# Kernel optimization log

Hardware: AMD Instinct MI355X
Metric: run time of the kernel (lower is better)

## Reference

```python
import jax, jax.numpy as jnp
import numpy as np

Y_SCALE = 0.01  # fixed weight quantization scale (q_scale of the int8 weights)


def setup_inputs() -> dict:
    key = jax.random.key(0)
    kx, kw, kb = jax.random.split(key, 3)
    B, S, IN, OUT = 4, 2048, 4096, 4096
    x = jax.random.normal(kx, (B, S, IN), dtype=jnp.float32)
    # int8 quantized weights, stored transposed as (in_features, out_features)
    weight_q = jax.random.randint(kw, (IN, OUT), -128, 128, dtype=jnp.int32)
    bias = jax.random.normal(kb, (OUT,), dtype=jnp.float32)
    return {"x": x, "weight_q": weight_q, "bias": bias}


def reference(x, weight_q, bias):
    # Per-batch-sample dynamic activation scale: max(|x_i|)/128 over each [S, IN] slice
    x_scale = jnp.max(jnp.abs(x), axis=(1, 2), keepdims=True) / 128.0  # [B,1,1]
    # int8 quantize: round + clip
    xq = jnp.clip(jnp.round(x / x_scale), -128, 127).astype(jnp.int8)  # [B,S,IN]
    wq = weight_q.astype(jnp.int8)                                      # [IN,OUT]
    c = jax.lax.dot_general(
        xq, wq,
        dimension_numbers=(((2,), (0,)), ((), ())),
        preferred_element_type=jnp.int32,
    )  # [B,S,OUT]
    # dequantize and bias-add
    y = c.astype(jnp.float32) * (x_scale * Y_SCALE)
    return y + bias
```

## Files before the change

kernel.cpp:

```cpp
#include <hip/hip_runtime.h>
#include <stdint.h>

#define K_DIM 4096
#define N_DIM 4096
#define M_DIM 8192
#define S_ROWS 2048
#define NT 32

typedef int v4i __attribute__((ext_vector_type(4)));

__device__ __forceinline__ void gload16(const void* g, void* l) {
    __builtin_amdgcn_global_load_lds(
        (const __attribute__((address_space(1))) unsigned int*)g,
        (__attribute__((address_space(3))) unsigned int*)l, 16, 0, 0);
}

__device__ __forceinline__ void barrier() {
    asm volatile("" ::: "memory");
    __builtin_amdgcn_s_barrier();
    asm volatile("" ::: "memory");
}

__global__ void prep1_kernel(const float* __restrict__ x, unsigned* __restrict__ amax,
                             const int* __restrict__ wq, char* __restrict__ wt) {
    __shared__ unsigned lds[64 * 17];
    if (blockIdx.x < 4096) {
        int b = blockIdx.x >> 10;
        int bx = blockIdx.x & 1023;
        const float4* xb = (const float4*)(x + (size_t)b * S_ROWS * K_DIM);
        int tid = bx * 256 + threadIdx.x;
        const int stride = 1024 * 256;
        float m = 0.f;
#pragma unroll
        for (int i = 0; i < 8; ++i) {
            float4 v = xb[tid + i * stride];
            m = fmaxf(m, fmaxf(fmaxf(fabsf(v.x), fabsf(v.y)),
                               fmaxf(fabsf(v.z), fabsf(v.w))));
        }
#pragma unroll
        for (int off = 32; off; off >>= 1)
            m = fmaxf(m, __shfl_xor(m, off));
        float* red = (float*)lds;
        if ((threadIdx.x & 63) == 0) red[threadIdx.x >> 6] = m;
        __syncthreads();
        if (threadIdx.x == 0) {
            m = fmaxf(fmaxf(red[0], red[1]), fmaxf(red[2], red[3]));
            atomicMax(&amax[b], __float_as_uint(m));
        }
    } else {
        int wb = blockIdx.x - 4096;
        int n0 = (wb & 63) * 64;
        int k0 = (wb >> 6) * 64;
        int t = threadIdx.x;
        int c = t & 63;
        int g = t >> 6;
#pragma unroll
        for (int rep = 0; rep < 4; ++rep) {
            int kb = g * 16 + rep * 4;
            int v0 = wq[(size_t)(k0 + kb + 0) * N_DIM + n0 + c];
            int v1 = wq[(size_t)(k0 + kb + 1) * N_DIM + n0 + c];
            int v2 = wq[(size_t)(k0 + kb + 2) * N_DIM + n0 + c];
            int v3 = wq[(size_t)(k0 + kb + 3) * N_DIM + n0 + c];
            lds[c * 17 + (kb >> 2)] =
                (v0 & 255) | ((v1 & 255) << 8) | ((v2 & 255) << 16) | ((v3 & 255) << 24);
        }
        __syncthreads();
        int row = t >> 2;
        int ch = t & 3;
        uint4 o;
        o.x = lds[row * 17 + ch * 4 + 0];
        o.y = lds[row * 17 + ch * 4 + 1];
        o.z = lds[row * 17 + ch * 4 + 2];
        o.w = lds[row * 17 + ch * 4 + 3];
        *(uint4*)(wt + (size_t)(n0 + row) * K_DIM + k0 + ch * 16) = o;
    }
}

__global__ void quant_kernel(const float* __restrict__ x,
                             const unsigned* __restrict__ amax,
                             char* __restrict__ xq) {
    size_t gid = (size_t)blockIdx.x * 256 + threadIdx.x;
    size_t base = gid * 16;
    int b = (int)(base >> 23);
    float inv = 128.0f / __uint_as_float(amax[b]);
    const float4* xs = (const float4*)(x + base);
    unsigned parts[4];
#pragma unroll
    for (int i = 0; i < 4; ++i) {
        float4 v = xs[i];
        int q0 = max(-128, min(127, (int)rintf(v.x * inv)));
        int q1 = max(-128, min(127, (int)rintf(v.y * inv)));
        int q2 = max(-128, min(127, (int)rintf(v.z * inv)));
        int q3 = max(-128, min(127, (int)rintf(v.w * inv)));
        parts[i] = (q0 & 255) | ((q1 & 255) << 8) | ((q2 & 255) << 16) | ((q3 & 255) << 24);
    }
    *(uint4*)(xq + base) = make_uint4(parts[0], parts[1], parts[2], parts[3]);
}

__global__ __launch_bounds__(512, 2) void gemm8_kernel(
    const char* __restrict__ A, const char* __restrict__ Bt,
    const float* __restrict__ bias, const unsigned* __restrict__ amax,
    float* __restrict__ out) {
    __shared__ char sm[131072];
    const int t = threadIdx.x;
    const int l = t & 63;
    const int w = t >> 6;
    const int wm = w >> 2;
    const int wn = w & 3;
    const int rb = l & 15;
    const int sg = l >> 4;

    int bid = blockIdx.x;
    int swz = (bid & 7) * 64 + (bid >> 3);
    int mt = swz >> 4, nt = swz & 15;
    const size_t m0 = (size_t)mt * 256;
    const size_t n0 = (size_t)nt * 256;

    const int s0 = (sg ^ (rb & 7)) << 4;
    const int s1 = s0 ^ 64;
    const int baseA = (wm * 128 + rb) * 128;
    const int baseB = 32768 + (wn * 64 + rb) * 128;

    v4i acc[8][4];
#pragma unroll
    for (int i = 0; i < 8; ++i)
#pragma unroll
        for (int j = 0; j < 4; ++j) acc[i][j] = (v4i){0, 0, 0, 0};

#define ST_FULL(tt)                                                          \
    if ((tt) < NT) {                                                         \
        char* lb = sm + (((tt) & 1) << 16);                                  \
        const char* ga = A + m0 * K_DIM + (size_t)(tt) * 128;                \
        const char* gb = Bt + n0 * K_DIM + (size_t)(tt) * 128;               \
        _Pragma("unroll")                                                    \
        for (int j = 0; j < 4; ++j) {                                        \
            int p = j * 512 + t;                                             \
            int r = p >> 3, sl = p & 7;                                      \
            int s = sl ^ (r & 7);                                            \
            gload16(ga + (size_t)r * K_DIM + s * 16, lb + p * 16);           \
        }                                                                    \
        _Pragma("unroll")                                                    \
        for (int j = 0; j < 4; ++j) {                                        \
            int p = j * 512 + t;                                             \
            int r = p >> 3, sl = p & 7;                                      \
            int s = sl ^ (r & 7);                                            \
            gload16(gb + (size_t)r * K_DIM + s * 16, lb + 32768 + p * 16);   \
        }                                                                    \
    }

#define MFMA_PAIR(accrow, afrag)                                             \
    _Pragma("unroll")                                                        \
    for (int ni = 0; ni < 4; ++ni)                                           \
        _Pragma("unroll")                                                    \
        for (int ks = 0; ks < 2; ++ks)                                       \
            acc[accrow][ni] = __builtin_amdgcn_mfma_i32_16x16x64_i8(         \
                afrag[ks], bF[ni][ks], acc[accrow][ni], 0, 0, 0);

    ST_FULL(0);

    v4i aP[2][2], bF[4][2];

    for (int i = 0; i < NT; ++i) {
        const char* pb = sm + ((i & 1) << 16);
        const char* pA0 = pb + baseA + s0;
        const char* pA1 = pb + baseA + s1;
        const char* pB0 = pb + baseB + s0;
        const char* pB1 = pb + baseB + s1;

        barrier();
        ST_FULL(i + 1);
        if (i == NT - 1) { asm volatile("s_waitcnt vmcnt(0)" ::: "memory"); }
        else             { asm volatile("s_waitcnt vmcnt(8)" ::: "memory"); }
        barrier();

#pragma unroll
        for (int ni = 0; ni < 4; ++ni) {
            bF[ni][0] = *(const v4i*)(pB0 + ni * 2048);
            bF[ni][1] = *(const v4i*)(pB1 + ni * 2048);
        }
        aP[0][0] = *(const v4i*)(pA0 + 0 * 2048); aP[0][1] = *(const v4i*)(pA1 + 0 * 2048);
        aP[1][0] = *(const v4i*)(pA0 + 1 * 2048); aP[1][1] = *(const v4i*)(pA1 + 1 * 2048);
        __builtin_amdgcn_s_setprio(1);
        MFMA_PAIR(0, aP[0]); MFMA_PAIR(1, aP[1]);
        aP[0][0] = *(const v4i*)(pA0 + 2 * 2048); aP[0][1] = *(const v4i*)(pA1 + 2 * 2048);
        aP[1][0] = *(const v4i*)(pA0 + 3 * 2048); aP[1][1] = *(const v4i*)(pA1 + 3 * 2048);
        MFMA_PAIR(2, aP[0]); MFMA_PAIR(3, aP[1]);
        aP[0][0] = *(const v4i*)(pA0 + 0 * 2048 + 8192); aP[0][1] = *(const v4i*)(pA1 + 0 * 2048 + 8192);
        aP[1][0] = *(const v4i*)(pA0 + 1 * 2048 + 8192); aP[1][1] = *(const v4i*)(pA1 + 1 * 2048 + 8192);
        MFMA_PAIR(4, aP[0]); MFMA_PAIR(5, aP[1]);
        aP[0][0] = *(const v4i*)(pA0 + 2 * 2048 + 8192); aP[0][1] = *(const v4i*)(pA1 + 2 * 2048 + 8192);
        aP[1][0] = *(const v4i*)(pA0 + 3 * 2048 + 8192); aP[1][1] = *(const v4i*)(pA1 + 3 * 2048 + 8192);
        MFMA_PAIR(6, aP[0]); MFMA_PAIR(7, aP[1]);
        __builtin_amdgcn_s_setprio(0);
    }

    float scale = __uint_as_float(amax[m0 >> 11]) * (1.0f / 128.0f) * 0.01f;
    float bv[4];
#pragma unroll
    for (int ni = 0; ni < 4; ++ni) bv[ni] = bias[n0 + wn * 64 + ni * 16 + rb];
#pragma unroll
    for (int mi = 0; mi < 8; ++mi) {
#pragma unroll
        for (int rg = 0; rg < 4; ++rg) {
            size_t row = m0 + wm * 128 + mi * 16 + sg * 4 + rg;
            float* orow = out + row * N_DIM + n0 + wn * 64 + rb;
#pragma unroll
            for (int ni = 0; ni < 4; ++ni)
                orow[ni * 16] = (float)acc[mi][ni][rg] * scale + bv[ni];
        }
    }
#undef ST_FULL
#undef MFMA_PAIR
}

extern "C" void kernel_launch(void* const* d_in, const int* in_sizes, int n_in,
                              void* d_out, int out_size, void* d_ws, size_t ws_size,
                              hipStream_t stream) {
    const float* x = (const float*)d_in[0];
    const int* wq = (const int*)d_in[1];
    const float* bias = (const float*)d_in[2];
    float* out = (float*)d_out;

    unsigned* amax = (unsigned*)d_ws;
    char* xq = (char*)d_ws + 256;
    char* wt = (char*)d_ws + 256 + (size_t)M_DIM * K_DIM;

    hipMemsetAsync(d_ws, 0, 16, stream);

    prep1_kernel<<<dim3(8192), 256, 0, stream>>>(x, amax, wq, wt);
    quant_kernel<<<8192, 256, 0, stream>>>(x, amax, xq);
    gemm8_kernel<<<dim3(512), 512, 0, stream>>>(xq, wt, bias, amax, out);
}
```

Measured before the change: 225.2 us.

## Pre-swizzle weights into MFMA fragment layout and load B directly to registers

The weight transpose kernel now writes B in a fragment-packed layout, so each lane can load its MFMA B operands straight from global memory into registers. This removes B from LDS, which halves shared memory to 64KB, and double-buffers B in registers (bP/bQ) across a two-step unrolled loop. The block-to-tile mapping is changed so each XCD covers two N tiles across all M. The cost is higher register pressure and full vmcnt(0) waits each step, which may expose global-load latency that was previously hidden.

Result: slower. 229.9 us (+2.1%).

```diff
diff --git a/kernel.cpp b/kernel.cpp
--- a/kernel.cpp
+++ b/kernel.cpp
@@ -20,6 +20,7 @@
     __builtin_amdgcn_s_barrier();
     asm volatile("" ::: "memory");
 }
+
 
 __global__ void prep1_kernel(const float* __restrict__ x, unsigned* __restrict__ amax,
                              const int* __restrict__ wq, char* __restrict__ wt) {
@@ -50,17 +51,17 @@
     } else {
         int wb = blockIdx.x - 4096;
         int n0 = (wb & 63) * 64;
-        int k0 = (wb >> 6) * 64;
+        int k0b = (wb >> 6) * 64;
         int t = threadIdx.x;
         int c = t & 63;
         int g = t >> 6;
 #pragma unroll
         for (int rep = 0; rep < 4; ++rep) {
             int kb = g * 16 + rep * 4;
-            int v0 = wq[(size_t)(k0 + kb + 0) * N_DIM + n0 + c];
-            int v1 = wq[(size_t)(k0 + kb + 1) * N_DIM + n0 + c];
-            int v2 = wq[(size_t)(k0 + kb + 2) * N_DIM + n0 + c];
-            int v3 = wq[(size_t)(k0 + kb + 3) * N_DIM + n0 + c];
+            int v0 = wq[(size_t)(k0b + kb + 0) * N_DIM + n0 + c];
+            int v1 = wq[(size_t)(k0b + kb + 1) * N_DIM + n0 + c];
+            int v2 = wq[(size_t)(k0b + kb + 2) * N_DIM + n0 + c];
+            int v3 = wq[(size_t)(k0b + kb + 3) * N_DIM + n0 + c];
             lds[c * 17 + (kb >> 2)] =
                 (v0 & 255) | ((v1 & 255) << 8) | ((v2 & 255) << 16) | ((v3 & 255) << 24);
         }
@@ -72,7 +73,11 @@
         o.y = lds[row * 17 + ch * 4 + 1];
         o.z = lds[row * 17 + ch * 4 + 2];
         o.w = lds[row * 17 + ch * 4 + 3];
-        *(uint4*)(wt + (size_t)(n0 + row) * K_DIM + k0 + ch * 16) = o;
+        int n = n0 + row;
+        int k0 = k0b + ch * 16;
+        size_t dst = ((size_t)(n >> 4) * 64 + (k0 >> 6)) * 1024 +
+                     (size_t)((n & 15) + ((k0 >> 4) & 3) * 16) * 16;
+        *(uint4*)(wt + dst) = o;
     }
 }
 
@@ -101,7 +106,7 @@
     const char* __restrict__ A, const char* __restrict__ Bt,
     const float* __restrict__ bias, const unsigned* __restrict__ amax,
     float* __restrict__ out) {
-    __shared__ char sm[131072];
+    __shared__ char sm[65536];
     const int t = threadIdx.x;
     const int l = t & 63;
     const int w = t >> 6;
@@ -111,15 +116,18 @@
     const int sg = l >> 4;
 
     int bid = blockIdx.x;
-    int swz = (bid & 7) * 64 + (bid >> 3);
-    int mt = swz >> 4, nt = swz & 15;
+    int xcd = bid & 7;
+    int idx = bid >> 3;
+    int nt = (xcd << 1) | (idx & 1);
+    int mt = idx >> 1;
     const size_t m0 = (size_t)mt * 256;
     const size_t n0 = (size_t)nt * 256;
 
     const int s0 = (sg ^ (rb & 7)) << 4;
     const int s1 = s0 ^ 64;
     const int baseA = (wm * 128 + rb) * 128;
-    const int baseB = 32768 + (wn * 64 + rb) * 128;
+
+    const char* bBase = Bt + (((size_t)(n0 >> 4) + wn * 4) * 64) * 1024 + l * 16;
 
     v4i acc[8][4];
 #pragma unroll
@@ -127,11 +135,10 @@
 #pragma unroll
         for (int j = 0; j < 4; ++j) acc[i][j] = (v4i){0, 0, 0, 0};
 
-#define ST_FULL(tt)                                                          \
+#define ST_A(tt)                                                             \
     if ((tt) < NT) {                                                         \
-        char* lb = sm + (((tt) & 1) << 16);                                  \
+        char* lb = sm + (((tt) & 1) << 15);                                  \
         const char* ga = A + m0 * K_DIM + (size_t)(tt) * 128;                \
-        const char* gb = Bt + n0 * K_DIM + (size_t)(tt) * 128;               \
         _Pragma("unroll")                                                    \
         for (int j = 0; j < 4; ++j) {                                        \
             int p = j * 512 + t;                                             \
@@ -139,59 +146,72 @@
             int s = sl ^ (r & 7);                                            \
             gload16(ga + (size_t)r * K_DIM + s * 16, lb + p * 16);           \
         }                                                                    \
-        _Pragma("unroll")                                                    \
-        for (int j = 0; j < 4; ++j) {                                        \
-            int p = j * 512 + t;                                             \
-            int r = p >> 3, sl = p & 7;                                      \
-            int s = sl ^ (r & 7);                                            \
-            gload16(gb + (size_t)r * K_DIM + s * 16, lb + 32768 + p * 16);   \
-        }                                                                    \
-    }
-
-#define MFMA_PAIR(accrow, afrag)                                             \
-    _Pragma("unroll")                                                        \
-    for (int ni = 0; ni < 4; ++ni)                                           \
-        _Pragma("unroll")                                                    \
-        for (int ks = 0; ks < 2; ++ks)                                       \
-            acc[accrow][ni] = __builtin_amdgcn_mfma_i32_16x16x64_i8(         \
-                afrag[ks], bF[ni][ks], acc[accrow][ni], 0, 0, 0);
-
-    ST_FULL(0);
-
-    v4i aP[2][2], bF[4][2];
-
-    for (int i = 0; i < NT; ++i) {
-        const char* pb = sm + ((i & 1) << 16);
-        const char* pA0 = pb + baseA + s0;
-        const char* pA1 = pb + baseA + s1;
-        const char* pB0 = pb + baseB + s0;
-        const char* pB1 = pb + baseB + s1;
-
+    }
+
+#define LDB(buf, tt)                                                         \
+    {                                                                        \
+        int tc = (tt) < NT ? (tt) : (NT - 1);                                \
+        _Pragma("unroll")                                                    \
+        for (int ni = 0; ni < 4; ++ni) {                                     \
+            buf[ni][0] = *(const v4i*)(bBase + ni * 65536 + (size_t)(tc * 2) * 1024);     \
+            buf[ni][1] = *(const v4i*)(bBase + ni * 65536 + (size_t)(tc * 2 + 1) * 1024); \
+        }                                                                    \
+    }
+
+#define COMPUTE(i, bCur)                                                     \
+    {                                                                        \
+        const char* pb = sm + (((i) & 1) << 15);                             \
+        const char* pA0 = pb + baseA + s0;                                   \
+        const char* pA1 = pb + baseA + s1;                                   \
+        _Pragma("unroll")                                                    \
+        for (int mi = 0; mi < 4; ++mi) {                                     \
+            aF[mi][0] = *(const v4i*)(pA0 + mi * 2048);                      \
+            aF[mi][1] = *(const v4i*)(pA1 + mi * 2048);                      \
+        }                                                                    \
+        __builtin_amdgcn_s_setprio(1);                                       \
+        _Pragma("unroll")                                                    \
+        for (int mi = 0; mi < 4; ++mi)                                       \
+            _Pragma("unroll")                                                \
+            for (int ni = 0; ni < 4; ++ni)                                   \
+                _Pragma("unroll")                                            \
+                for (int ks = 0; ks < 2; ++ks)                               \
+                    acc[mi][ni] = __builtin_amdgcn_mfma_i32_16x16x64_i8(     \
+                        aF[mi][ks], bCur[ni][ks], acc[mi][ni], 0, 0, 0);     \
+        __builtin_amdgcn_s_setprio(0);                                       \
+        _Pragma("unroll")                                                    \
+        for (int mi = 0; mi < 4; ++mi) {                                     \
+            aF[mi][0] = *(const v4i*)(pA0 + mi * 2048 + 8192);               \
+            aF[mi][1] = *(const v4i*)(pA1 + mi * 2048 + 8192);               \
+        }                                                                    \
+        __builtin_amdgcn_s_setprio(1);                                       \
+        _Pragma("unroll")                                                    \
+        for (int mi = 0; mi < 4; ++mi)                                       \
+            _Pragma("unroll")                                                \
+            for (int ni = 0; ni < 4; ++ni)                                   \
+                _Pragma("unroll")                                            \
+                for (int ks = 0; ks < 2; ++ks)                               \
+                    acc[mi + 4][ni] = __builtin_amdgcn_mfma_i32_16x16x64_i8( \
+                        aF[mi][ks], bCur[ni][ks], acc[mi + 4][ni], 0, 0, 0); \
+        __builtin_amdgcn_s_setprio(0);                                       \
+    }
+
+    v4i aF[4][2], bP[4][2], bQ[4][2];
+
+    ST_A(0);
+    LDB(bP, 0);
+
+    for (int i = 0; i < NT; i += 2) {
+        asm volatile("s_waitcnt vmcnt(0)" ::: "memory");
         barrier();
-        ST_FULL(i + 1);
-        if (i == NT - 1) { asm volatile("s_waitcnt vmcnt(0)" ::: "memory"); }
-        else             { asm volatile("s_waitcnt vmcnt(8)" ::: "memory"); }
+        ST_A(i + 1);
+        LDB(bQ, i + 1);
+        COMPUTE(i, bP);
+
+        asm volatile("s_waitcnt vmcnt(0)" ::: "memory");
         barrier();
-
-#pragma unroll
-        for (int ni = 0; ni < 4; ++ni) {
-            bF[ni][0] = *(const v4i*)(pB0 + ni * 2048);
-            bF[ni][1] = *(const v4i*)(pB1 + ni * 2048);
-        }
-        aP[0][0] = *(const v4i*)(pA0 + 0 * 2048); aP[0][1] = *(const v4i*)(pA1 + 0 * 2048);
-        aP[1][0] = *(const v4i*)(pA0 + 1 * 2048); aP[1][1] = *(const v4i*)(pA1 + 1 * 2048);
-        __builtin_amdgcn_s_setprio(1);
-        MFMA_PAIR(0, aP[0]); MFMA_PAIR(1, aP[1]);
-        aP[0][0] = *(const v4i*)(pA0 + 2 * 2048); aP[0][1] = *(const v4i*)(pA1 + 2 * 2048);
-        aP[1][0] = *(const v4i*)(pA0 + 3 * 2048); aP[1][1] = *(const v4i*)(pA1 + 3 * 2048);
-        MFMA_PAIR(2, aP[0]); MFMA_PAIR(3, aP[1]);
-        aP[0][0] = *(const v4i*)(pA0 + 0 * 2048 + 8192); aP[0][1] = *(const v4i*)(pA1 + 0 * 2048 + 8192);
-        aP[1][0] = *(const v4i*)(pA0 + 1 * 2048 + 8192); aP[1][1] = *(const v4i*)(pA1 + 1 * 2048 + 8192);
-        MFMA_PAIR(4, aP[0]); MFMA_PAIR(5, aP[1]);
-        aP[0][0] = *(const v4i*)(pA0 + 2 * 2048 + 8192); aP[0][1] = *(const v4i*)(pA1 + 2 * 2048 + 8192);
-        aP[1][0] = *(const v4i*)(pA0 + 3 * 2048 + 8192); aP[1][1] = *(const v4i*)(pA1 + 3 * 2048 + 8192);
-        MFMA_PAIR(6, aP[0]); MFMA_PAIR(7, aP[1]);
-        __builtin_amdgcn_s_setprio(0);
+        ST_A(i + 2);
+        LDB(bP, i + 2);
+        COMPUTE(i + 1, bQ);
     }
 
     float scale = __uint_as_float(amax[m0 >> 11]) * (1.0f / 128.0f) * 0.01f;
@@ -209,8 +229,9 @@
                 orow[ni * 16] = (float)acc[mi][ni][rg] * scale + bv[ni];
         }
     }
-#undef ST_FULL
-#undef MFMA_PAIR
+#undef ST_A
+#undef LDB
+#undef COMPUTE
 }
 
 extern "C" void kernel_launch(void* const* d_in, const int* in_sizes, int n_in,
```
